# Kernel tuning notes

Hardware: AMD Instinct MI355X
Metric: run time of the kernel (lower is better)

The kernel has to match this reference:

```python
import jax, jax.numpy as jnp
import numpy as np

N_NODES = 50000
N_EDGES = 800000
D_IN, D_H1, D_H2 = 256, 128, 64


def setup_inputs() -> dict:
    key = jax.random.key(0)
    k1, k2, k3, k4, k5, k6, k7 = jax.random.split(key, 7)
    x = jax.random.normal(k1, (N_NODES, D_IN), dtype=jnp.float32)
    edge_index = jax.random.randint(k2, (2, N_EDGES), 0, N_NODES, dtype=jnp.int64)
    edge_weight = jax.random.uniform(k3, (N_EDGES,), dtype=jnp.float32)
    # GCNConv params: Linear (no bias) weight + separate bias, Glorot-ish scale
    W1 = jax.random.normal(k4, (D_IN, D_H1), dtype=jnp.float32) / np.sqrt(D_IN)
    b1 = jnp.zeros((D_H1,), dtype=jnp.float32)
    W2 = jax.random.normal(k5, (D_H1, D_H2), dtype=jnp.float32) / np.sqrt(D_H1)
    b2 = jnp.zeros((D_H2,), dtype=jnp.float32)
    return {"x": x, "edge_index": edge_index, "edge_weight": edge_weight,
            "W1": W1, "b1": b1, "W2": W2, "b2": b2}


def _gcn_norm(edge_index, edge_weight, n_nodes):
    # PyG gcn_norm: add self-loops (weight 1), symmetric D^-1/2 A D^-1/2
    loops = jnp.arange(n_nodes, dtype=edge_index.dtype)
    src = jnp.concatenate([edge_index[0], loops])
    dst = jnp.concatenate([edge_index[1], loops])
    w = jnp.concatenate([edge_weight, jnp.ones((n_nodes,), edge_weight.dtype)])
    deg = jax.ops.segment_sum(w, dst, num_segments=n_nodes)
    dinv = jnp.where(deg > 0, jax.lax.rsqrt(deg), 0.0)
    norm = dinv[src] * w * dinv[dst]  # [E+N]
    return src, dst, norm


def _gcn_conv(h, src, dst, norm, W, b, n_nodes):
    h = h @ W                                   # [N, d_out] dense GEMM
    msg = h[src] * norm[:, None]                # gather + scale  [E+N, d_out]
    out = jax.ops.segment_sum(msg, dst, num_segments=n_nodes)  # scatter-add
    return out + b


def reference(x, edge_index, edge_weight, W1, b1, W2, b2):
    n = x.shape[0]
    src, dst, norm = _gcn_norm(edge_index, edge_weight, n)
    # dropout p=0 -> identity
    h = jax.nn.relu(_gcn_conv(x, src, dst, norm, W1, b1, n))
    h = jax.nn.relu(_gcn_conv(h, src, dst, norm, W2, b2, n))
    return h
```

## Files before the change

kernel.cpp:

```cpp
#include <hip/hip_runtime.h>


static constexpr int SCAN_CHUNK = 1024;

using short8 = __attribute__((ext_vector_type(8))) short;
using f32x4  = __attribute__((ext_vector_type(4))) float;

__device__ inline unsigned short bf16rne(float f) {
  unsigned u = __float_as_uint(f);
  u += 0x7fffu + ((u >> 16) & 1u);
  return (unsigned short)(u >> 16);
}
__device__ inline float bflo(unsigned u) { return __uint_as_float(u << 16); }
__device__ inline float bfhi(unsigned u) { return __uint_as_float(u & 0xffff0000u); }

__global__ __launch_bounds__(256) void k_zero(int* __restrict__ p, int n) {
  int i = blockIdx.x * 256 + threadIdx.x;
  if (i < n) p[i] = 0;
}

__global__ __launch_bounds__(256) void k_count(const int* __restrict__ dst,
                                               int* __restrict__ cnt,
                                               int* __restrict__ epos, int E) {
  int e = blockIdx.x * 256 + threadIdx.x;
  if (e < E) epos[e] = atomicAdd(&cnt[dst[e]], 1);
}

__global__ __launch_bounds__(256) void k_scan1(const int* __restrict__ in,
                                               int* __restrict__ out,
                                               int* __restrict__ sums, int n) {
  __shared__ int sd[256];
  const int base = blockIdx.x * SCAN_CHUNK;
  const int tid = threadIdx.x;
  int v[4], tot = 0;
#pragma unroll
  for (int j = 0; j < 4; ++j) {
    int idx = base + tid * 4 + j;
    v[j] = (idx < n) ? in[idx] : 0;
    tot += v[j];
  }
  sd[tid] = tot;
  __syncthreads();
  for (int d = 1; d < 256; d <<= 1) {
    int t = (tid >= d) ? sd[tid - d] : 0;
    __syncthreads();
    sd[tid] += t;
    __syncthreads();
  }
  if (tid == 255) sums[blockIdx.x] = sd[255];
  int run = sd[tid] - tot;
#pragma unroll
  for (int j = 0; j < 4; ++j) {
    int idx = base + tid * 4 + j;
    if (idx < n) out[idx] = run;
    run += v[j];
  }
}

__global__ __launch_bounds__(64) void k_scan2(int* __restrict__ sums, int n) {
  int tid = threadIdx.x;
  int o = (tid < n) ? sums[tid] : 0;
  int v = o;
  for (int d = 1; d < 64; d <<= 1) {
    int t = __shfl_up(v, d, 64);
    if (tid >= d) v += t;
  }
  if (tid < n) sums[tid] = v - o;
}

__global__ __launch_bounds__(256) void k_scan3(int* __restrict__ out,
                                               const int* __restrict__ sums, int n) {
  const int base = blockIdx.x * SCAN_CHUNK;
  const int add = sums[blockIdx.x];
  for (int j = threadIdx.x; j < SCAN_CHUNK; j += 256) {
    int idx = base + j;
    if (idx < n) out[idx] += add;
  }
}

__global__ __launch_bounds__(256) void k_bucket2(const int* __restrict__ src,
                                                 const int* __restrict__ dst,
                                                 const float* __restrict__ w,
                                                 const int* __restrict__ row_ptr,
                                                 const int* __restrict__ epos,
                                                 int2* __restrict__ csr, int E) {
  int e = blockIdx.x * 256 + threadIdx.x;
  if (e < E) {
    int d = dst[e];
    csr[row_ptr[d] + epos[e]] = make_int2(src[e], __float_as_int(w[e]));
  }
}

__global__ __launch_bounds__(256) void k_deg_dinv(const int* __restrict__ row_ptr,
                                                  const int2* __restrict__ csr,
                                                  float* __restrict__ dinv, int n) {
  int i = blockIdx.x * 256 + threadIdx.x;
  if (i >= n) return;
  const int e0 = row_ptr[i], e1 = row_ptr[i + 1];
  float s = 1.0f;
  int e = e0;
  for (; e + 4 <= e1; e += 4) {
    float w0 = __int_as_float(csr[e].y), w1 = __int_as_float(csr[e + 1].y);
    float w2 = __int_as_float(csr[e + 2].y), w3 = __int_as_float(csr[e + 3].y);
    s += (w0 + w1) + (w2 + w3);
  }
  for (; e < e1; ++e) s += __int_as_float(csr[e].y);
  dinv[i] = rsqrtf(s);
}

template <int K, int C>
__global__ __launch_bounds__(256) void k_wtp(const float* __restrict__ W,
                                             unsigned short* __restrict__ Wtp) {
  constexpr int NT = C / 16;
  int i = blockIdx.x * 256 + threadIdx.x;
  if (i >= K * C) return;
  int e = i & 7;
  int l = (i >> 3) & 63;
  int rest = i >> 9;
  int nt = rest % NT;
  int kc = rest / NT;
  int k = kc * 32 + (l >> 4) * 8 + e;
  int n = nt * 16 + (l & 15);
  Wtp[i] = bf16rne(W[(size_t)k * C + n]);
}

template <int K, int C, bool A_F32>
__global__ __launch_bounds__(256, 2) void k_gemm_mfma(
    const void* __restrict__ Aptr, const unsigned short* __restrict__ Wtp,
    const float* __restrict__ dinv, unsigned short* __restrict__ H, int n) {
  constexpr int NT = C / 16;
  constexpr int KCH = K / 32;
  const int w = threadIdx.x >> 6;
  const int l = threadIdx.x & 63;
  const int lm = l & 15;
  const int lk = (l >> 4) * 8;
  const int row0 = (blockIdx.x * 4 + w) * 16;
  if (row0 >= n) return;
  const int m = row0 + lm;
  const bool valid = m < n;
  const size_t arow = (size_t)(valid ? m : 0) * K;

  short8 af[KCH];
  if (A_F32) {
    const float* A = (const float*)Aptr;
    float4 a[2 * KCH];
#pragma unroll
    for (int c = 0; c < KCH; ++c) {
      if (valid) {
        a[2 * c]     = *(const float4*)(A + arow + c * 32 + lk);
        a[2 * c + 1] = *(const float4*)(A + arow + c * 32 + lk + 4);
      } else {
        a[2 * c] = a[2 * c + 1] = make_float4(0.f, 0.f, 0.f, 0.f);
      }
    }
#pragma unroll
    for (int c = 0; c < KCH; ++c) {
      af[c][0] = (short)bf16rne(a[2 * c].x);     af[c][1] = (short)bf16rne(a[2 * c].y);
      af[c][2] = (short)bf16rne(a[2 * c].z);     af[c][3] = (short)bf16rne(a[2 * c].w);
      af[c][4] = (short)bf16rne(a[2 * c + 1].x); af[c][5] = (short)bf16rne(a[2 * c + 1].y);
      af[c][6] = (short)bf16rne(a[2 * c + 1].z); af[c][7] = (short)bf16rne(a[2 * c + 1].w);
    }
  } else {
    const unsigned short* A = (const unsigned short*)Aptr;
#pragma unroll
    for (int c = 0; c < KCH; ++c)
      af[c] = valid ? *(const short8*)(A + arow + c * 32 + lk)
                    : short8{0, 0, 0, 0, 0, 0, 0, 0};
  }

  f32x4 acc[NT] = {};
  const short8* B = (const short8*)Wtp;
#pragma unroll
  for (int c = 0; c < KCH; ++c)
#pragma unroll
    for (int nt = 0; nt < NT; ++nt)
      acc[nt] = __builtin_amdgcn_mfma_f32_16x16x32_bf16(af[c], B[(c * NT + nt) * 64 + l],
                                                        acc[nt], 0, 0, 0);

  const int orow = row0 + (l >> 4) * 4;
  float dv[4];
#pragma unroll
  for (int r = 0; r < 4; ++r) dv[r] = (orow + r < n) ? dinv[orow + r] : 0.f;
#pragma unroll
  for (int nt = 0; nt < NT; ++nt) {
#pragma unroll
    for (int r = 0; r < 4; ++r) {
      int g = orow + r;
      if (g < n) H[(size_t)g * C + nt * 16 + lm] = bf16rne(acc[nt][r] * dv[r]);
    }
  }
}

template <int C, bool OUTF32>
__global__ __launch_bounds__(256) void k_aggregate(
    const int* __restrict__ row_ptr, const int2* __restrict__ csr,
    const unsigned short* __restrict__ h, const float* __restrict__ dinv,
    const float* __restrict__ bias, void* __restrict__ outp, int n) {
  constexpr int LPE = C / 4;
  constexpr int NPB = 256 / LPE;
  const int g = threadIdx.x % LPE;
  const int i = blockIdx.x * NPB + threadIdx.x / LPE;
  if (i >= n) return;
  const uint2* h2 = (const uint2*)h;
  uint2 hv = h2[(size_t)i * LPE + g];
  float a0 = bflo(hv.x), a1 = bfhi(hv.x);
  float a2 = bflo(hv.y), a3 = bfhi(hv.y);
  const int e1 = row_ptr[i + 1];
  int e = row_ptr[i];
  for (; e + 8 <= e1; e += 8) {
    int2 c[8];
    uint2 v[8];
#pragma unroll
    for (int j = 0; j < 8; ++j) c[j] = csr[e + j];
#pragma unroll
    for (int j = 0; j < 8; ++j) v[j] = h2[(size_t)c[j].x * LPE + g];
#pragma unroll
    for (int j = 0; j < 8; ++j) {
      float wj = __int_as_float(c[j].y);
      a0 = fmaf(bflo(v[j].x), wj, a0); a1 = fmaf(bfhi(v[j].x), wj, a1);
      a2 = fmaf(bflo(v[j].y), wj, a2); a3 = fmaf(bfhi(v[j].y), wj, a3);
    }
  }
  for (; e + 4 <= e1; e += 4) {
    int2 c[4];
    uint2 v[4];
#pragma unroll
    for (int j = 0; j < 4; ++j) c[j] = csr[e + j];
#pragma unroll
    for (int j = 0; j < 4; ++j) v[j] = h2[(size_t)c[j].x * LPE + g];
#pragma unroll
    for (int j = 0; j < 4; ++j) {
      float wj = __int_as_float(c[j].y);
      a0 = fmaf(bflo(v[j].x), wj, a0); a1 = fmaf(bfhi(v[j].x), wj, a1);
      a2 = fmaf(bflo(v[j].y), wj, a2); a3 = fmaf(bfhi(v[j].y), wj, a3);
    }
  }
  for (; e < e1; ++e) {
    int2 c = csr[e];
    float wj = __int_as_float(c.y);
    uint2 v = h2[(size_t)c.x * LPE + g];
    a0 = fmaf(bflo(v.x), wj, a0); a1 = fmaf(bfhi(v.x), wj, a1);
    a2 = fmaf(bflo(v.y), wj, a2); a3 = fmaf(bfhi(v.y), wj, a3);
  }
  const float di = dinv[i];
  float4 bb = ((const float4*)bias)[g];
  a0 = fmaxf(fmaf(a0, di, bb.x), 0.f);
  a1 = fmaxf(fmaf(a1, di, bb.y), 0.f);
  a2 = fmaxf(fmaf(a2, di, bb.z), 0.f);
  a3 = fmaxf(fmaf(a3, di, bb.w), 0.f);
  if (OUTF32) {
    ((float4*)outp)[(size_t)i * LPE + g] = make_float4(a0, a1, a2, a3);
  } else {
    uint2 o;
    o.x = (unsigned)bf16rne(a0) | ((unsigned)bf16rne(a1) << 16);
    o.y = (unsigned)bf16rne(a2) | ((unsigned)bf16rne(a3) << 16);
    ((uint2*)outp)[(size_t)i * LPE + g] = o;
  }
}

extern "C" void kernel_launch(void* const* d_in, const int* in_sizes, int n_in,
                              void* d_out, int out_size, void* d_ws, size_t ws_size,
                              hipStream_t stream) {
  (void)n_in; (void)out_size; (void)ws_size;
  const float* x  = (const float*)d_in[0];
  const int*   ei = (const int*)d_in[1];
  const float* ew = (const float*)d_in[2];
  const float* W1 = (const float*)d_in[3];
  const float* b1 = (const float*)d_in[4];
  const float* W2 = (const float*)d_in[5];
  const float* b2 = (const float*)d_in[6];
  float* out = (float*)d_out;

  const int N = in_sizes[0] / 256;
  const int E = in_sizes[2];
  const int* src = ei;
  const int* dst = ei + E;

  float* ws      = (float*)d_ws;
  float* dinv    = ws;
  int*   row_ptr = (int*)(ws + 50176);
  int*   cnt     = row_ptr + 50176;
  int*   chunks  = cnt + 50176;
  int*   epos    = chunks + 256;
  int2*  csr     = (int2*)(epos + 800256);
  unsigned short* h1   = (unsigned short*)((int*)csr + 2 * 800256);
  unsigned short* o1   = h1 + (size_t)50000 * 128;
  unsigned short* wtp1 = o1 + (size_t)50000 * 128;
  unsigned short* wtp2 = wtp1 + 128 * 256;
  unsigned short* h2   = h1;

  const int nb_e = (E + 255) / 256;
  const int nchunks = (N + 1 + SCAN_CHUNK - 1) / SCAN_CHUNK;

  k_zero<<<(N + 1 + 255) / 256, 256, 0, stream>>>(cnt, N + 1);
  k_count<<<nb_e, 256, 0, stream>>>(dst, cnt, epos, E);
  k_scan1<<<nchunks, 256, 0, stream>>>(cnt, row_ptr, chunks, N + 1);
  k_scan2<<<1, 64, 0, stream>>>(chunks, nchunks);
  k_scan3<<<nchunks, 256, 0, stream>>>(row_ptr, chunks, N + 1);
  k_bucket2<<<nb_e, 256, 0, stream>>>(src, dst, ew, row_ptr, epos, csr, E);
  k_deg_dinv<<<(N + 255) / 256, 256, 0, stream>>>(row_ptr, csr, dinv, N);

  k_wtp<256, 128><<<(256 * 128 + 255) / 256, 256, 0, stream>>>(W1, wtp1);
  k_wtp<128, 64><<<(128 * 64 + 255) / 256, 256, 0, stream>>>(W2, wtp2);

  k_gemm_mfma<256, 128, true><<<(N + 63) / 64, 256, 0, stream>>>(x, wtp1, dinv, h1, N);
  k_aggregate<128, false><<<(N + 7) / 8, 256, 0, stream>>>(row_ptr, csr, h1, dinv,
                                                           b1, o1, N);
  k_gemm_mfma<128, 64, false><<<(N + 63) / 64, 256, 0, stream>>>(o1, wtp2, dinv, h2, N);
  k_aggregate<64, true><<<(N + 15) / 16, 256, 0, stream>>>(row_ptr, csr, h2, dinv,
                                                           b2, out, N);
}
```

Before: 161.6 us.

## Fuse weight packing into zero kernel, widen aggregate gathers, raise GEMM occupancy

The zeroing kernel and both weight-packing kernels are merged into one prep launch, removing two kernel launches. The aggregate kernel now has each lane gather 16 bytes (8 bf16) per edge instead of 8, which halves the lanes per node and doubles nodes per block. GEMM launch bounds ask for 3 or 4 waves per SIMD instead of 2, which may force register spills. Wider gathers mean fewer memory instructions, but there are fewer lanes in flight per edge fetch.

```diff
diff --git a/kernel.cpp b/kernel.cpp
--- a/kernel.cpp
+++ b/kernel.cpp
@@ -14,9 +14,29 @@
 __device__ inline float bflo(unsigned u) { return __uint_as_float(u << 16); }
 __device__ inline float bfhi(unsigned u) { return __uint_as_float(u & 0xffff0000u); }
 
-__global__ __launch_bounds__(256) void k_zero(int* __restrict__ p, int n) {
+__device__ inline void wtp_pack(const float* __restrict__ W,
+                                unsigned short* __restrict__ Wtp,
+                                int i, int K, int C) {
+  int e = i & 7;
+  int l = (i >> 3) & 63;
+  int rest = i >> 9;
+  int NT = C / 16;
+  int nt = rest % NT;
+  int kc = rest / NT;
+  int k = kc * 32 + (l >> 4) * 8 + e;
+  int n = nt * 16 + (l & 15);
+  Wtp[i] = bf16rne(W[(size_t)k * C + n]);
+}
+
+__global__ __launch_bounds__(256) void k_prep(int* __restrict__ cnt, int n1,
+                                              const float* __restrict__ W1,
+                                              unsigned short* __restrict__ wtp1,
+                                              const float* __restrict__ W2,
+                                              unsigned short* __restrict__ wtp2) {
   int i = blockIdx.x * 256 + threadIdx.x;
-  if (i < n) p[i] = 0;
+  if (i < n1) cnt[i] = 0;
+  if (i < 256 * 128) wtp_pack(W1, wtp1, i, 256, 128);
+  if (i < 128 * 64) wtp_pack(W2, wtp2, i, 128, 64);
 }
 
 __global__ __launch_bounds__(256) void k_count(const int* __restrict__ dst,
@@ -108,24 +128,8 @@
   dinv[i] = rsqrtf(s);
 }
 
-template <int K, int C>
-__global__ __launch_bounds__(256) void k_wtp(const float* __restrict__ W,
-                                             unsigned short* __restrict__ Wtp) {
-  constexpr int NT = C / 16;
-  int i = blockIdx.x * 256 + threadIdx.x;
-  if (i >= K * C) return;
-  int e = i & 7;
-  int l = (i >> 3) & 63;
-  int rest = i >> 9;
-  int nt = rest % NT;
-  int kc = rest / NT;
-  int k = kc * 32 + (l >> 4) * 8 + e;
-  int n = nt * 16 + (l & 15);
-  Wtp[i] = bf16rne(W[(size_t)k * C + n]);
-}
-
 template <int K, int C, bool A_F32>
-__global__ __launch_bounds__(256, 2) void k_gemm_mfma(
+__global__ __launch_bounds__(256, A_F32 ? 3 : 4) void k_gemm_mfma(
     const void* __restrict__ Aptr, const unsigned short* __restrict__ Wtp,
     const float* __restrict__ dinv, unsigned short* __restrict__ H, int n) {
   constexpr int NT = C / 16;
@@ -196,65 +200,76 @@
     const int* __restrict__ row_ptr, const int2* __restrict__ csr,
     const unsigned short* __restrict__ h, const float* __restrict__ dinv,
     const float* __restrict__ bias, void* __restrict__ outp, int n) {
-  constexpr int LPE = C / 4;
-  constexpr int NPB = 256 / LPE;
-  const int g = threadIdx.x % LPE;
-  const int i = blockIdx.x * NPB + threadIdx.x / LPE;
+  constexpr int LPN = C / 8;
+  constexpr int NPB = 256 / LPN;
+  const int g = threadIdx.x % LPN;
+  const int i = blockIdx.x * NPB + threadIdx.x / LPN;
   if (i >= n) return;
-  const uint2* h2 = (const uint2*)h;
-  uint2 hv = h2[(size_t)i * LPE + g];
-  float a0 = bflo(hv.x), a1 = bfhi(hv.x);
-  float a2 = bflo(hv.y), a3 = bfhi(hv.y);
+  const uint4* h4 = (const uint4*)h;
+  uint4 hv = h4[(size_t)i * LPN + g];
+  float a0 = bflo(hv.x), a1 = bfhi(hv.x), a2 = bflo(hv.y), a3 = bfhi(hv.y);
+  float a4 = bflo(hv.z), a5 = bfhi(hv.z), a6 = bflo(hv.w), a7 = bfhi(hv.w);
   const int e1 = row_ptr[i + 1];
   int e = row_ptr[i];
   for (; e + 8 <= e1; e += 8) {
     int2 c[8];
-    uint2 v[8];
+    uint4 v[8];
 #pragma unroll
     for (int j = 0; j < 8; ++j) c[j] = csr[e + j];
 #pragma unroll
-    for (int j = 0; j < 8; ++j) v[j] = h2[(size_t)c[j].x * LPE + g];
+    for (int j = 0; j < 8; ++j) v[j] = h4[(size_t)c[j].x * LPN + g];
 #pragma unroll
     for (int j = 0; j < 8; ++j) {
       float wj = __int_as_float(c[j].y);
       a0 = fmaf(bflo(v[j].x), wj, a0); a1 = fmaf(bfhi(v[j].x), wj, a1);
       a2 = fmaf(bflo(v[j].y), wj, a2); a3 = fmaf(bfhi(v[j].y), wj, a3);
+      a4 = fmaf(bflo(v[j].z), wj, a4); a5 = fmaf(bfhi(v[j].z), wj, a5);
+      a6 = fmaf(bflo(v[j].w), wj, a6); a7 = fmaf(bfhi(v[j].w), wj, a7);
     }
   }
   for (; e + 4 <= e1; e += 4) {
     int2 c[4];
-    uint2 v[4];
+    uint4 v[4];
 #pragma unroll
     for (int j = 0; j < 4; ++j) c[j] = csr[e + j];
 #pragma unroll
-    for (int j = 0; j < 4; ++j) v[j] = h2[(size_t)c[j].x * LPE + g];
+    for (int j = 0; j < 4; ++j) v[j] = h4[(size_t)c[j].x * LPN + g];
 #pragma unroll
     for (int j = 0; j < 4; ++j) {
       float wj = __int_as_float(c[j].y);
       a0 = fmaf(bflo(v[j].x), wj, a0); a1 = fmaf(bfhi(v[j].x), wj, a1);
       a2 = fmaf(bflo(v[j].y), wj, a2); a3 = fmaf(bfhi(v[j].y), wj, a3);
+      a4 = fmaf(bflo(v[j].z), wj, a4); a5 = fmaf(bfhi(v[j].z), wj, a5);
+      a6 = fmaf(bflo(v[j].w), wj, a6); a7 = fmaf(bfhi(v[j].w), wj, a7);
     }
   }
   for (; e < e1; ++e) {
     int2 c = csr[e];
     float wj = __int_as_float(c.y);
-    uint2 v = h2[(size_t)c.x * LPE + g];
+    uint4 v = h4[(size_t)c.x * LPN + g];
     a0 = fmaf(bflo(v.x), wj, a0); a1 = fmaf(bfhi(v.x), wj, a1);
     a2 = fmaf(bflo(v.y), wj, a2); a3 = fmaf(bfhi(v.y), wj, a3);
+    a4 = fmaf(bflo(v.z), wj, a4); a5 = fmaf(bfhi(v.z), wj, a5);
+    a6 = fmaf(bflo(v.w), wj, a6); a7 = fmaf(bfhi(v.w), wj, a7);
   }
   const float di = dinv[i];
-  float4 bb = ((const float4*)bias)[g];
-  a0 = fmaxf(fmaf(a0, di, bb.x), 0.f);
-  a1 = fmaxf(fmaf(a1, di, bb.y), 0.f);
-  a2 = fmaxf(fmaf(a2, di, bb.z), 0.f);
-  a3 = fmaxf(fmaf(a3, di, bb.w), 0.f);
+  const float4* b4 = (const float4*)bias;
+  float4 bb0 = b4[g * 2], bb1 = b4[g * 2 + 1];
+  a0 = fmaxf(fmaf(a0, di, bb0.x), 0.f); a1 = fmaxf(fmaf(a1, di, bb0.y), 0.f);
+  a2 = fmaxf(fmaf(a2, di, bb0.z), 0.f); a3 = fmaxf(fmaf(a3, di, bb0.w), 0.f);
+  a4 = fmaxf(fmaf(a4, di, bb1.x), 0.f); a5 = fmaxf(fmaf(a5, di, bb1.y), 0.f);
+  a6 = fmaxf(fmaf(a6, di, bb1.z), 0.f); a7 = fmaxf(fmaf(a7, di, bb1.w), 0.f);
   if (OUTF32) {
-    ((float4*)outp)[(size_t)i * LPE + g] = make_float4(a0, a1, a2, a3);
+    float4* o4 = (float4*)outp;
+    o4[(size_t)i * (C / 4) + g * 2]     = make_float4(a0, a1, a2, a3);
+    o4[(size_t)i * (C / 4) + g * 2 + 1] = make_float4(a4, a5, a6, a7);
   } else {
-    uint2 o;
+    uint4 o;
     o.x = (unsigned)bf16rne(a0) | ((unsigned)bf16rne(a1) << 16);
     o.y = (unsigned)bf16rne(a2) | ((unsigned)bf16rne(a3) << 16);
-    ((uint2*)outp)[(size_t)i * LPE + g] = o;
+    o.z = (unsigned)bf16rne(a4) | ((unsigned)bf16rne(a5) << 16);
+    o.w = (unsigned)bf16rne(a6) | ((unsigned)bf16rne(a7) << 16);
+    ((uint4*)outp)[(size_t)i * LPN + g] = o;
   }
 }
 
@@ -292,7 +307,7 @@
   const int nb_e = (E + 255) / 256;
   const int nchunks = (N + 1 + SCAN_CHUNK - 1) / SCAN_CHUNK;
 
-  k_zero<<<(N + 1 + 255) / 256, 256, 0, stream>>>(cnt, N + 1);
+  k_prep<<<(N + 1 + 255) / 256, 256, 0, stream>>>(cnt, N + 1, W1, wtp1, W2, wtp2);
   k_count<<<nb_e, 256, 0, stream>>>(dst, cnt, epos, E);
   k_scan1<<<nchunks, 256, 0, stream>>>(cnt, row_ptr, chunks, N + 1);
   k_scan2<<<1, 64, 0, stream>>>(chunks, nchunks);
@@ -300,13 +315,10 @@
   k_bucket2<<<nb_e, 256, 0, stream>>>(src, dst, ew, row_ptr, epos, csr, E);
   k_deg_dinv<<<(N + 255) / 256, 256, 0, stream>>>(row_ptr, csr, dinv, N);
 
-  k_wtp<256, 128><<<(256 * 128 + 255) / 256, 256, 0, stream>>>(W1, wtp1);
-  k_wtp<128, 64><<<(128 * 64 + 255) / 256, 256, 0, stream>>>(W2, wtp2);
-
   k_gemm_mfma<256, 128, true><<<(N + 63) / 64, 256, 0, stream>>>(x, wtp1, dinv, h1, N);
-  k_aggregate<128, false><<<(N + 7) / 8, 256, 0, stream>>>(row_ptr, csr, h1, dinv,
-                                                           b1, o1, N);
+  k_aggregate<128, false><<<(N + 15) / 16, 256, 0, stream>>>(row_ptr, csr, h1, dinv,
+                                                             b1, o1, N);
   k_gemm_mfma<128, 64, false><<<(N + 63) / 64, 256, 0, stream>>>(o1, wtp2, dinv, h2, N);
-  k_aggregate<64, true><<<(N + 15) / 16, 256, 0, stream>>>(row_ptr, csr, h2, dinv,
+  k_aggregate<64, true><<<(N + 31) / 32, 256, 0, stream>>>(row_ptr, csr, h2, dinv,
                                                            b2, out, N);
 }
```

Result: faster. 157.8 us (-2.4%).
